# Performance work log

Hardware: AMD Instinct MI355X
Metric: run time of the kernel (lower is better)

Reference implementation:

```python
import jax, jax.numpy as jnp
import numpy as np


def setup_inputs() -> dict:
    key = jax.random.key(0)
    k1, k2 = jax.random.split(key)
    from_points = jax.random.normal(k1, (16384, 64), dtype=jnp.float32)
    to_points = jax.random.normal(k2, (16384, 64), dtype=jnp.float32)
    return {"from_points": from_points, "to_points": to_points}


def reference(from_points, to_points):
    # Squared L2 distance matrix [N, M] via ||a||^2 + ||b||^2 - 2 a.b,
    # avoiding the O(N*M*D) broadcasted intermediate of the original.
    a_sq = jnp.sum(from_points * from_points, axis=-1)          # [N]
    b_sq = jnp.sum(to_points * to_points, axis=-1)              # [M]
    cross = jnp.einsum('nd,md->nm', from_points, to_points)     # [N, M]
    dist_mat = a_sq[:, None] + b_sq[None, :] - 2.0 * cross      # [N, M]
    # Row-wise min (nearest neighbor squared distance), then sum.
    return jnp.sum(jnp.min(dist_mat, axis=1))
```

## Files before the change

### kernel.cpp

```cpp
#include <hip/hip_runtime.h>
#include <stdint.h>

#define N_PTS 16384
#define TSPLITS 32
#define TO_TILES 16
#define FGPB 16
#define NBLOCKS (TSPLITS * (256 / FGPB))

typedef __attribute__((ext_vector_type(4)))  int i32x4;
typedef __attribute__((ext_vector_type(16))) int i32x16;

__device__ __forceinline__ int imin(int a, int b) { return a < b ? a : b; }
__device__ __forceinline__ int itree16(i32x16 a) {
    int m0 = imin(imin(a[0],  a[1]),  a[2]);
    int m1 = imin(imin(a[3],  a[4]),  a[5]);
    int m2 = imin(imin(a[6],  a[7]),  a[8]);
    int m3 = imin(imin(a[9],  a[10]), a[11]);
    int m4 = imin(imin(a[12], a[13]), a[14]);
    int m5 = imin(imin(a[15], m0), m1);
    return imin(imin(imin(m2, m3), m4), m5);
}
__device__ __forceinline__ int q8(float x) {
    int q = __float2int_rn(x);
    return q < -127 ? -127 : (q > 127 ? 127 : q);
}

__global__ __launch_bounds__(256) void prep_kernel(
        const float* __restrict__ from_pts, const float* __restrict__ to_pts,
        float* __restrict__ a_sq, int* __restrict__ bsqi,
        char* __restrict__ BfQ, char* __restrict__ AtoQ,
        float* __restrict__ out) {
    int gid = blockIdx.x * 256 + threadIdx.x;
    int row = gid >> 3;
    int sub = gid & 7;
    bool isFrom = row < N_PTS;
    int r = row & (N_PTS - 1);
    const float* src = isFrom ? from_pts : to_pts;
    float4 v0 = ((const float4*)src)[r * 16 + sub * 2];
    float4 v1 = ((const float4*)src)[r * 16 + sub * 2 + 1];
    float s = v0.x*v0.x + v0.y*v0.y + v0.z*v0.z + v0.w*v0.w
            + v1.x*v1.x + v1.y*v1.y + v1.z*v1.z + v1.w*v1.w;
    s += __shfl_xor(s, 1); s += __shfl_xor(s, 2); s += __shfl_xor(s, 4);
    float sc = isFrom ? -16.0f : 16.0f;
    int q0 = q8(v0.x*sc), q1 = q8(v0.y*sc), q2 = q8(v0.z*sc), q3 = q8(v0.w*sc);
    int q4 = q8(v1.x*sc), q5 = q8(v1.y*sc), q6 = q8(v1.z*sc), q7 = q8(v1.w*sc);
    int2 w;
    w.x = (q0 & 255) | ((q1 & 255) << 8) | ((q2 & 255) << 16) | (q3 << 24);
    w.y = (q4 & 255) | ((q5 & 255) << 8) | ((q6 & 255) << 16) | (q7 << 24);
    int st = r >> 5;
    int m  = r & 31;
    int kb = sub >> 2, h = (sub >> 1) & 1, half8 = sub & 1;
    size_t off = (((size_t)st * 2 + kb) * 64 + h * 32 + m) * 16 + 8 * half8;
    if (isFrom) {
        *(int2*)(BfQ + off) = w;
        if (sub == 0) a_sq[r] = s;
    } else {
        *(int2*)(AtoQ + off) = w;
        if (sub == 0)
            bsqi[st * 32 + ((m >> 2) & 1) * 16 + (m & 3) + 4 * (m >> 3)] =
                __float2int_rn(128.0f * s);
    }
    if (gid == 0) out[0] = 0.0f;
}

__global__ __launch_bounds__(512, 4) void main_kernel(
        const char* __restrict__ BfQ, const char* __restrict__ AtoQ,
        const int* __restrict__ bsqi, int* __restrict__ pmin) {
    __shared__ __align__(16) char abuf[32768];

    const int tid = threadIdx.x;
    const int lane = tid & 63;
    const int l31 = lane & 31;
    const int h   = lane >> 5;
    const int wv  = tid >> 6;
    const int ts  = blockIdx.x >> 4;
    const int bg  = blockIdx.x & 15;
    const int gtb = ts * TO_TILES;

    #pragma unroll
    for (int j2 = 0; j2 < 4; j2++) {
        int j = wv * 4 + j2;
        const char* g = AtoQ +
            (((size_t)(gtb + (j >> 1)) * 2 + (j & 1)) * 64 + lane) * 16;
        char* l = &abuf[j * 1024];
        __builtin_amdgcn_global_load_lds(
            (const __attribute__((address_space(1))) unsigned int*)g,
            (__attribute__((address_space(3))) unsigned int*)l, 16, 0, 0);
    }
    __syncthreads();

    const int fgA = bg * FGPB + wv;
    const int fgB = fgA + 8;
    i32x4 B00[2], B01[2], B10[2], B11[2];
    #pragma unroll
    for (int kb = 0; kb < 2; kb++) {
        B00[kb] = *(const i32x4*)(BfQ + (((size_t)(2 * fgA)     * 2 + kb) * 64 + lane) * 16);
        B01[kb] = *(const i32x4*)(BfQ + (((size_t)(2 * fgA + 1) * 2 + kb) * 64 + lane) * 16);
        B10[kb] = *(const i32x4*)(BfQ + (((size_t)(2 * fgB)     * 2 + kb) * 64 + lane) * 16);
        B11[kb] = *(const i32x4*)(BfQ + (((size_t)(2 * fgB + 1) * 2 + kb) * 64 + lane) * 16);
    }
    int rmin00 = 0x7FFFFFFF, rmin01 = 0x7FFFFFFF;
    int rmin10 = 0x7FFFFFFF, rmin11 = 0x7FFFFFFF;

    #define LOADT(T, A, CU)                                                     \
        {                                                                       \
            int t_ = (T);                                                       \
            A[0] = *(const i32x4*)&abuf[((t_ * 2 + 0) * 64 + lane) * 16];       \
            A[1] = *(const i32x4*)&abuf[((t_ * 2 + 1) * 64 + lane) * 16];       \
            const int4* cp_ = (const int4*)(bsqi + (gtb + t_) * 32 + h * 16);   \
            union { int4 f[4]; i32x16 v; } cu_;                                 \
            cu_.f[0] = cp_[0]; cu_.f[1] = cp_[1];                               \
            cu_.f[2] = cp_[2]; cu_.f[3] = cp_[3];                               \
            CU = cu_.v;                                                         \
        }
    #define DOT(A, CU)                                                          \
        {                                                                       \
            i32x16 c0 = __builtin_amdgcn_mfma_i32_32x32x32_i8(A[0], B00[0], CU, 0, 0, 0); \
            i32x16 c1 = __builtin_amdgcn_mfma_i32_32x32x32_i8(A[0], B01[0], CU, 0, 0, 0); \
            c0 = __builtin_amdgcn_mfma_i32_32x32x32_i8(A[1], B00[1], c0, 0, 0, 0); \
            c1 = __builtin_amdgcn_mfma_i32_32x32x32_i8(A[1], B01[1], c1, 0, 0, 0); \
            rmin00 = imin(rmin00, itree16(c0));                                 \
            rmin01 = imin(rmin01, itree16(c1));                                 \
            i32x16 c2 = __builtin_amdgcn_mfma_i32_32x32x32_i8(A[0], B10[0], CU, 0, 0, 0); \
            i32x16 c3 = __builtin_amdgcn_mfma_i32_32x32x32_i8(A[0], B11[0], CU, 0, 0, 0); \
            c2 = __builtin_amdgcn_mfma_i32_32x32x32_i8(A[1], B10[1], c2, 0, 0, 0); \
            c3 = __builtin_amdgcn_mfma_i32_32x32x32_i8(A[1], B11[1], c3, 0, 0, 0); \
            rmin10 = imin(rmin10, itree16(c2));                                 \
            rmin11 = imin(rmin11, itree16(c3));                                 \
        }

    i32x4 Aa[2], Ab[2];
    i32x16 cua, cub;
    LOADT(0, Aa, cua)
    #pragma unroll 1
    for (int t = 0; t < TO_TILES; t += 2) {
        LOADT(t + 1, Ab, cub)
        DOT(Aa, cua)
        LOADT((t + 2) & (TO_TILES - 1), Aa, cua)
        DOT(Ab, cub)
    }

    rmin00 = imin(rmin00, __shfl_xor(rmin00, 32));
    rmin01 = imin(rmin01, __shfl_xor(rmin01, 32));
    rmin10 = imin(rmin10, __shfl_xor(rmin10, 32));
    rmin11 = imin(rmin11, __shfl_xor(rmin11, 32));
    if (lane < 32) {
        pmin[(size_t)ts * N_PTS + fgA * 64 + l31]      = rmin00;
        pmin[(size_t)ts * N_PTS + fgA * 64 + 32 + l31] = rmin01;
        pmin[(size_t)ts * N_PTS + fgB * 64 + l31]      = rmin10;
        pmin[(size_t)ts * N_PTS + fgB * 64 + 32 + l31] = rmin11;
    }
}

__global__ __launch_bounds__(256) void finish_kernel(
        const float* __restrict__ a_sq, const int* __restrict__ pmin,
        float* __restrict__ out) {
    int r = blockIdx.x * 256 + threadIdx.x;
    int m = pmin[r];
    #pragma unroll
    for (int s = 1; s < TSPLITS; s++)
        m = imin(m, pmin[(size_t)s * N_PTS + r]);
    float v = a_sq[r] + (float)m * 0.0078125f;
    #pragma unroll
    for (int k = 1; k < 64; k <<= 1) v += __shfl_xor(v, k);
    __shared__ float red[4];
    if ((threadIdx.x & 63) == 0) red[threadIdx.x >> 6] = v;
    __syncthreads();
    if (threadIdx.x == 0)
        atomicAdd(out, red[0] + red[1] + red[2] + red[3]);
}

extern "C" void kernel_launch(void* const* d_in, const int* in_sizes, int n_in,
                              void* d_out, int out_size, void* d_ws, size_t ws_size,
                              hipStream_t stream) {
    const float* from_pts = (const float*)d_in[0];
    const float* to_pts   = (const float*)d_in[1];
    char* ws = (char*)d_ws;
    float* a_sq = (float*)ws;
    int*   bsqi = (int*)(ws + (64 << 10));
    int*   pmin = (int*)(ws + (128 << 10));
    char*  BfQ  = ws + (128 << 10) + (2 << 20);
    char*  AtoQ = ws + (128 << 10) + (3 << 20);

    prep_kernel<<<(2 * N_PTS * 8) / 256, 256, 0, stream>>>(
        from_pts, to_pts, a_sq, bsqi, BfQ, AtoQ, (float*)d_out);
    main_kernel<<<NBLOCKS, 512, 0, stream>>>(BfQ, AtoQ, bsqi, pmin);
    finish_kernel<<<N_PTS / 256, 256, 0, stream>>>(a_sq, pmin, (float*)d_out);
}
```

Baseline: 78.61 us.

## Stage bsq in LDS, raise MFMA priority, and reduce row minima with atomicMin

```diff
diff --git a/kernel.cpp b/kernel.cpp
--- a/kernel.cpp
+++ b/kernel.cpp
@@ -29,8 +29,9 @@
         const float* __restrict__ from_pts, const float* __restrict__ to_pts,
         float* __restrict__ a_sq, int* __restrict__ bsqi,
         char* __restrict__ BfQ, char* __restrict__ AtoQ,
-        float* __restrict__ out) {
+        int* __restrict__ pmin16, float* __restrict__ out) {
     int gid = blockIdx.x * 256 + threadIdx.x;
+    if (gid < N_PTS) pmin16[gid] = 0x7FFFFFFF;
     int row = gid >> 3;
     int sub = gid & 7;
     bool isFrom = row < N_PTS;
@@ -65,8 +66,8 @@
 
 __global__ __launch_bounds__(512, 4) void main_kernel(
         const char* __restrict__ BfQ, const char* __restrict__ AtoQ,
-        const int* __restrict__ bsqi, int* __restrict__ pmin) {
-    __shared__ __align__(16) char abuf[32768];
+        const int* __restrict__ bsqi, int* __restrict__ pmin16) {
+    __shared__ __align__(16) char abuf[32768 + 2048];
 
     const int tid = threadIdx.x;
     const int lane = tid & 63;
@@ -87,6 +88,16 @@
             (const __attribute__((address_space(1))) unsigned int*)g,
             (__attribute__((address_space(3))) unsigned int*)l, 16, 0, 0);
     }
+    if (wv == 0) {
+        #pragma unroll
+        for (int j = 0; j < 2; j++) {
+            const int* g = bsqi + gtb * 32 + j * 256 + lane * 4;
+            char* l = &abuf[32768 + j * 1024];
+            __builtin_amdgcn_global_load_lds(
+                (const __attribute__((address_space(1))) unsigned int*)g,
+                (__attribute__((address_space(3))) unsigned int*)l, 16, 0, 0);
+        }
+    }
     __syncthreads();
 
     const int fgA = bg * FGPB + wv;
@@ -107,14 +118,17 @@
             int t_ = (T);                                                       \
             A[0] = *(const i32x4*)&abuf[((t_ * 2 + 0) * 64 + lane) * 16];       \
             A[1] = *(const i32x4*)&abuf[((t_ * 2 + 1) * 64 + lane) * 16];       \
-            const int4* cp_ = (const int4*)(bsqi + (gtb + t_) * 32 + h * 16);   \
-            union { int4 f[4]; i32x16 v; } cu_;                                 \
-            cu_.f[0] = cp_[0]; cu_.f[1] = cp_[1];                               \
-            cu_.f[2] = cp_[2]; cu_.f[3] = cp_[3];                               \
+            const char* cb_ = &abuf[32768 + t_ * 128 + h * 64];                 \
+            union { i32x4 f[4]; i32x16 v; } cu_;                                \
+            cu_.f[0] = *(const i32x4*)(cb_ + 0);                                \
+            cu_.f[1] = *(const i32x4*)(cb_ + 16);                               \
+            cu_.f[2] = *(const i32x4*)(cb_ + 32);                               \
+            cu_.f[3] = *(const i32x4*)(cb_ + 48);                               \
             CU = cu_.v;                                                         \
         }
     #define DOT(A, CU)                                                          \
         {                                                                       \
+            __builtin_amdgcn_s_setprio(1);                                      \
             i32x16 c0 = __builtin_amdgcn_mfma_i32_32x32x32_i8(A[0], B00[0], CU, 0, 0, 0); \
             i32x16 c1 = __builtin_amdgcn_mfma_i32_32x32x32_i8(A[0], B01[0], CU, 0, 0, 0); \
             c0 = __builtin_amdgcn_mfma_i32_32x32x32_i8(A[1], B00[1], c0, 0, 0, 0); \
@@ -125,6 +139,7 @@
             i32x16 c3 = __builtin_amdgcn_mfma_i32_32x32x32_i8(A[0], B11[0], CU, 0, 0, 0); \
             c2 = __builtin_amdgcn_mfma_i32_32x32x32_i8(A[1], B10[1], c2, 0, 0, 0); \
             c3 = __builtin_amdgcn_mfma_i32_32x32x32_i8(A[1], B11[1], c3, 0, 0, 0); \
+            __builtin_amdgcn_s_setprio(0);                                      \
             rmin10 = imin(rmin10, itree16(c2));                                 \
             rmin11 = imin(rmin11, itree16(c3));                                 \
         }
@@ -145,22 +160,18 @@
     rmin10 = imin(rmin10, __shfl_xor(rmin10, 32));
     rmin11 = imin(rmin11, __shfl_xor(rmin11, 32));
     if (lane < 32) {
-        pmin[(size_t)ts * N_PTS + fgA * 64 + l31]      = rmin00;
-        pmin[(size_t)ts * N_PTS + fgA * 64 + 32 + l31] = rmin01;
-        pmin[(size_t)ts * N_PTS + fgB * 64 + l31]      = rmin10;
-        pmin[(size_t)ts * N_PTS + fgB * 64 + 32 + l31] = rmin11;
+        atomicMin(&pmin16[fgA * 64 + l31],      rmin00);
+        atomicMin(&pmin16[fgA * 64 + 32 + l31], rmin01);
+        atomicMin(&pmin16[fgB * 64 + l31],      rmin10);
+        atomicMin(&pmin16[fgB * 64 + 32 + l31], rmin11);
     }
 }
 
 __global__ __launch_bounds__(256) void finish_kernel(
-        const float* __restrict__ a_sq, const int* __restrict__ pmin,
+        const float* __restrict__ a_sq, const int* __restrict__ pmin16,
         float* __restrict__ out) {
     int r = blockIdx.x * 256 + threadIdx.x;
-    int m = pmin[r];
-    #pragma unroll
-    for (int s = 1; s < TSPLITS; s++)
-        m = imin(m, pmin[(size_t)s * N_PTS + r]);
-    float v = a_sq[r] + (float)m * 0.0078125f;
+    float v = a_sq[r] + (float)pmin16[r] * 0.0078125f;
     #pragma unroll
     for (int k = 1; k < 64; k <<= 1) v += __shfl_xor(v, k);
     __shared__ float red[4];
@@ -176,14 +187,14 @@
     const float* from_pts = (const float*)d_in[0];
     const float* to_pts   = (const float*)d_in[1];
     char* ws = (char*)d_ws;
-    float* a_sq = (float*)ws;
-    int*   bsqi = (int*)(ws + (64 << 10));
-    int*   pmin = (int*)(ws + (128 << 10));
-    char*  BfQ  = ws + (128 << 10) + (2 << 20);
-    char*  AtoQ = ws + (128 << 10) + (3 << 20);
+    float* a_sq   = (float*)ws;
+    int*   bsqi   = (int*)(ws + (64 << 10));
+    int*   pmin16 = (int*)(ws + (128 << 10));
+    char*  BfQ    = ws + (256 << 10);
+    char*  AtoQ   = ws + (256 << 10) + (1 << 20);
 
     prep_kernel<<<(2 * N_PTS * 8) / 256, 256, 0, stream>>>(
-        from_pts, to_pts, a_sq, bsqi, BfQ, AtoQ, (float*)d_out);
-    main_kernel<<<NBLOCKS, 512, 0, stream>>>(BfQ, AtoQ, bsqi, pmin);
-    finish_kernel<<<N_PTS / 256, 256, 0, stream>>>(a_sq, pmin, (float*)d_out);
-}
+        from_pts, to_pts, a_sq, bsqi, BfQ, AtoQ, pmin16, (float*)d_out);
+    main_kernel<<<NBLOCKS, 512, 0, stream>>>(BfQ, AtoQ, bsqi, pmin16);
+    finish_kernel<<<N_PTS / 256, 256, 0, stream>>>(a_sq, pmin16, (float*)d_out);
+}
```

New measurement: 77.57 us. No clear change (-1.3%).
